# Optimization experiments

Measured on AMD Instinct MI355X. Metric: run time of the kernel, lower is better.

## Reference

```python
import jax, jax.numpy as jnp
import numpy as np

B = 16384      # batch
H = 1024       # latent_dim
C = 2          # output_dim (classes)
PPC = 24       # prototypes per class
P = C * PPC    # 48 total prototypes
EPS = 1e-4


def setup_inputs() -> dict:
    key = jax.random.key(0)
    k1, k2, k3, k4, k5 = jax.random.split(key, 5)
    specific_user = jax.random.normal(k1, (B, H), jnp.float32)
    shared_user = jax.random.normal(k2, (B, H), jnp.float32)
    prototype_vectors = jax.random.normal(k3, (P, H), jnp.float32)
    # last_layer weight set by set_last_layer_incorrect_connection(-0.5):
    # +1 for the prototype's own class, -0.5 elsewhere; shape [C, P]
    cls = np.arange(P) // PPC
    ident = (cls[None, :] == np.arange(C)[:, None]).astype(np.float32)
    last_layer_w = jnp.asarray(ident * 1.0 + (1.0 - ident) * (-0.5))
    # nn.Bilinear(H, H, 1): weight [1, H, H], bias [1]
    bilinear_w = jax.random.normal(k4, (1, H, H), jnp.float32) / np.sqrt(H)
    bilinear_b = jax.random.normal(k5, (1,), jnp.float32) * 0.01
    return {
        "specific_user": specific_user,
        "shared_user": shared_user,
        "prototype_vectors": prototype_vectors,
        "last_layer_w": last_layer_w,
        "bilinear_w": bilinear_w,
        "bilinear_b": bilinear_b,
        "flag": 1,
    }


def reference(specific_user, shared_user, prototype_vectors, last_layer_w,
              bilinear_w, bilinear_b, flag):
    # prototype_distances: squared euclid via mm + norms, then log-similarity
    x2 = jnp.sum(specific_user ** 2, axis=1, keepdims=True)          # [B,1]
    p2 = jnp.sum(prototype_vectors ** 2, axis=1)                     # [P]
    distance = -2.0 * (specific_user @ prototype_vectors.T) + x2 + p2[None, :]  # [B,P]
    similarity = jnp.log((distance + 1.0) / (distance + EPS))        # [B,P]
    logits = similarity @ last_layer_w.T                             # [B,C]

    # select the class's 24 prototypes (flag picks class 1 or 0; static int)
    idx = 1 if flag else 0
    sub = prototype_vectors.reshape(C, PPC, H)[idx]                  # [PPC,H]

    # prototype_subgraph_distances: per original broadcast, each row of
    # all_sim is the batch-mean of the log-similarity -> constant over batch.
    s2 = jnp.sum(sub ** 2, axis=1)                                   # [PPC]
    d = -2.0 * (specific_user @ sub.T) + x2 + s2[None, :]            # [B,PPC]
    sim = jnp.mean(jnp.log((d + 1.0) / (d + EPS)), axis=0)           # [PPC]
    jstar = jnp.argmax(sim)                                          # scalar
    chosen_proto = jnp.broadcast_to(sub[jstar], specific_user.shape) # [B,H]

    # nn.Bilinear(chosen_proto, shared_user) -> [B,1]
    pos = jnp.einsum('bi,ij,bj->b', chosen_proto, bilinear_w[0], shared_user)[:, None] + bilinear_b
    return (pos, shared_user, logits, distance)
```

## Files before the change

### kernel.cpp

```cpp
#include <hip/hip_runtime.h>
#include <hip/hip_bf16.h>

#define BATCH 16384
#define HD    1024
#define NP    48
#define PPC   24
#define EPSV  1e-4f

typedef __attribute__((ext_vector_type(8))) short  short8;
typedef __attribute__((ext_vector_type(4))) float  floatx4;

__device__ __forceinline__ float b2f(unsigned short s) {
    union { unsigned u; float f; } c; c.u = ((unsigned)s) << 16; return c.f;
}
__device__ __forceinline__ unsigned short f2bu(float f) {
    __hip_bfloat16 h = __float2bfloat16(f);
    union { __hip_bfloat16 h; unsigned short u; } c; c.h = h; return c.u;
}

__global__ __launch_bounds__(64) void k_prep(const float* __restrict__ proto,
                                             unsigned short* __restrict__ phi,
                                             unsigned short* __restrict__ plo,
                                             float* __restrict__ p2) {
    const int p = blockIdx.x;
    const int lane = threadIdx.x;
    const float* row = proto + (size_t)p * HD;
    float acc = 0.f;
    for (int k = lane; k < HD; k += 64) {
        const float f = row[k];
        acc += f * f;
        const unsigned short h = f2bu(f);
        phi[(size_t)p * HD + k] = h;
        plo[(size_t)p * HD + k] = f2bu(f - b2f(h));
    }
#pragma unroll
    for (int m = 32; m >= 1; m >>= 1) acc += __shfl_xor(acc, m, 64);
    if (lane == 0) p2[p] = acc;
}

__global__ __launch_bounds__(256, 4) void k_main(
    const float* __restrict__ x,
    const unsigned short* __restrict__ phi,
    const unsigned short* __restrict__ plo,
    const float* __restrict__ llw,
    const float* __restrict__ p2,
    float* __restrict__ gcol,
    float* __restrict__ out_logits,
    float* __restrict__ out_dist)
{
    __shared__ float lacc[4][64][13];
    __shared__ float lx2[4][16];
    const int wave = threadIdx.x >> 6;
    const int lane = threadIdx.x & 63;
    const int quad = lane >> 4;
    const int lr   = lane & 15;
    const int rb   = blockIdx.x * 16;
    const int ko   = wave * 256;

    const float* xr = x + (size_t)(rb + lr) * HD + ko + quad * 8;
    const unsigned short* ph0 = phi + (size_t)lr * HD + ko + quad * 8;
    const unsigned short* ph1 = ph0 + 16 * HD;
    const unsigned short* ph2 = ph0 + 32 * HD;
    const unsigned short* pl0 = plo + (size_t)lr * HD + ko + quad * 8;
    const unsigned short* pl1 = pl0 + 16 * HD;
    const unsigned short* pl2 = pl0 + 32 * HD;

    floatx4 acc0 = {0.f, 0.f, 0.f, 0.f};
    floatx4 acc1 = {0.f, 0.f, 0.f, 0.f};
    floatx4 acc2 = {0.f, 0.f, 0.f, 0.f};
    float x2p = 0.f;

#pragma unroll 2
    for (int kk = 0; kk < 8; ++kk) {
        const floatx4 xa = *(const floatx4*)(xr + kk * 32);
        const floatx4 xb = *(const floatx4*)(xr + kk * 32 + 4);
        short8 ah, al;
#pragma unroll
        for (int j = 0; j < 4; ++j) {
            const float f = xa[j];
            x2p += f * f;
            const unsigned short h = f2bu(f);
            ah[j] = (short)h;
            al[j] = (short)f2bu(f - b2f(h));
        }
#pragma unroll
        for (int j = 0; j < 4; ++j) {
            const float f = xb[j];
            x2p += f * f;
            const unsigned short h = f2bu(f);
            ah[4 + j] = (short)h;
            al[4 + j] = (short)f2bu(f - b2f(h));
        }
        const short8 bh0 = *(const short8*)(ph0 + kk * 32);
        const short8 bh1 = *(const short8*)(ph1 + kk * 32);
        const short8 bh2 = *(const short8*)(ph2 + kk * 32);
        const short8 bl0 = *(const short8*)(pl0 + kk * 32);
        const short8 bl1 = *(const short8*)(pl1 + kk * 32);
        const short8 bl2 = *(const short8*)(pl2 + kk * 32);
        acc0 = __builtin_amdgcn_mfma_f32_16x16x32_bf16(ah, bh0, acc0, 0, 0, 0);
        acc0 = __builtin_amdgcn_mfma_f32_16x16x32_bf16(ah, bl0, acc0, 0, 0, 0);
        acc0 = __builtin_amdgcn_mfma_f32_16x16x32_bf16(al, bh0, acc0, 0, 0, 0);
        acc1 = __builtin_amdgcn_mfma_f32_16x16x32_bf16(ah, bh1, acc1, 0, 0, 0);
        acc1 = __builtin_amdgcn_mfma_f32_16x16x32_bf16(ah, bl1, acc1, 0, 0, 0);
        acc1 = __builtin_amdgcn_mfma_f32_16x16x32_bf16(al, bh1, acc1, 0, 0, 0);
        acc2 = __builtin_amdgcn_mfma_f32_16x16x32_bf16(ah, bh2, acc2, 0, 0, 0);
        acc2 = __builtin_amdgcn_mfma_f32_16x16x32_bf16(ah, bl2, acc2, 0, 0, 0);
        acc2 = __builtin_amdgcn_mfma_f32_16x16x32_bf16(al, bh2, acc2, 0, 0, 0);
    }
    x2p += __shfl_xor(x2p, 16, 64);
    x2p += __shfl_xor(x2p, 32, 64);

#pragma unroll
    for (int r = 0; r < 4; ++r) {
        lacc[wave][lane][r]     = acc0[r];
        lacc[wave][lane][4 + r] = acc1[r];
        lacc[wave][lane][8 + r] = acc2[r];
    }
    if (quad == 0) lx2[wave][lr] = x2p;
    __syncthreads();
    if (wave != 0) return;

    float facc[12];
#pragma unroll
    for (int i = 0; i < 12; ++i)
        facc[i] = lacc[0][lane][i] + lacc[1][lane][i] + lacc[2][lane][i] + lacc[3][lane][i];
    const float x2full = lx2[0][lr] + lx2[1][lr] + lx2[2][lr] + lx2[3][lr];

    float s0[4] = {0.f, 0.f, 0.f, 0.f};
    float s1[4] = {0.f, 0.f, 0.f, 0.f};

#pragma unroll
    for (int t = 0; t < 3; ++t) {
        const int p = t * 16 + lr;
        const float p2p = p2[p];
        const float w0 = llw[p];
        const float w1 = llw[NP + p];
        float cst = 0.f;
#pragma unroll
        for (int r = 0; r < 4; ++r) {
            const int row = quad * 4 + r;
            const float x2r = __shfl(x2full, row, 64);
            const float d = -2.f * facc[t * 4 + r] + x2r + p2p;
            out_dist[(size_t)(rb + row) * NP + p] = d;
            const float sim = log1pf((1.f - EPSV) / (d + EPSV));
            s0[r] += sim * w0;
            s1[r] += sim * w1;
            cst += sim;
        }
        cst += __shfl_xor(cst, 16, 64);
        cst += __shfl_xor(cst, 32, 64);
        if (quad == 0) atomicAdd(&gcol[p], cst);
    }

#pragma unroll
    for (int r = 0; r < 4; ++r) {
        float r0 = s0[r], r1 = s1[r];
#pragma unroll
        for (int m = 1; m <= 8; m <<= 1) {
            r0 += __shfl_xor(r0, m, 64);
            r1 += __shfl_xor(r1, m, 64);
        }
        if (lr == 0) {
            const int brow = rb + quad * 4 + r;
            out_logits[(size_t)brow * 2 + 0] = r0;
            out_logits[(size_t)brow * 2 + 1] = r1;
        }
    }
}

__global__ __launch_bounds__(256) void k_matvec(
    const float* __restrict__ proto,
    const float* __restrict__ w2,
    const float* __restrict__ gcol,
    const int* __restrict__ flag,
    float* __restrict__ v)
{
    __shared__ int js;
    const int tid = threadIdx.x;
    const int idx = (flag[0] != 0) ? 1 : 0;
    if (tid == 0) {
        const float* cs = gcol + idx * PPC;
        int bj = 0; float bv = cs[0];
        for (int j = 1; j < PPC; ++j)
            if (cs[j] > bv) { bv = cs[j]; bj = j; }
        js = bj;
    }
    __syncthreads();

    const float* crow = proto + (size_t)(idx * PPC + js) * HD;
    const int i0 = blockIdx.x * 16;
    const int j4 = tid * 4;
    float a0 = 0.f, a1 = 0.f, a2 = 0.f, a3 = 0.f;
#pragma unroll 4
    for (int i = i0; i < i0 + 16; ++i) {
        const float c = crow[i];
        const floatx4 wv = *(const floatx4*)(w2 + (size_t)i * HD + j4);
        a0 += c * wv[0];
        a1 += c * wv[1];
        a2 += c * wv[2];
        a3 += c * wv[3];
    }
    atomicAdd(&v[j4 + 0], a0);
    atomicAdd(&v[j4 + 1], a1);
    atomicAdd(&v[j4 + 2], a2);
    atomicAdd(&v[j4 + 3], a3);
}

__global__ __launch_bounds__(256) void k_pos(
    const float* __restrict__ sh,
    const float* __restrict__ v,
    const float* __restrict__ bias,
    float* __restrict__ out_pos,
    float* __restrict__ out_copy)
{
    const int wave = threadIdx.x >> 6;
    const int lane = threadIdx.x & 63;
    const int b = blockIdx.x * 4 + wave;

    const floatx4* src = (const floatx4*)(sh + (size_t)b * HD);
    floatx4* dst = (floatx4*)(out_copy + (size_t)b * HD);
    const floatx4* vv = (const floatx4*)v;
    float acc = 0.f;
#pragma unroll
    for (int c = 0; c < 4; ++c) {
        const int idx = c * 64 + lane;
        const floatx4 r = src[idx];
        __builtin_nontemporal_store(r, &dst[idx]);
        const floatx4 vr = vv[idx];
#pragma unroll
        for (int j = 0; j < 4; ++j) acc += r[j] * vr[j];
    }
#pragma unroll
    for (int m = 1; m <= 32; m <<= 1) acc += __shfl_xor(acc, m, 64);
    if (lane == 0) out_pos[b] = acc + bias[0];
}

extern "C" void kernel_launch(void* const* d_in, const int* in_sizes, int n_in,
                              void* d_out, int out_size, void* d_ws, size_t ws_size,
                              hipStream_t stream) {
    const float* x     = (const float*)d_in[0];
    const float* sh    = (const float*)d_in[1];
    const float* proto = (const float*)d_in[2];
    const float* llw   = (const float*)d_in[3];
    const float* w2    = (const float*)d_in[4];
    const float* bb    = (const float*)d_in[5];
    const int*   flag  = (const int*)d_in[6];

    float* out = (float*)d_out;
    float* out_pos    = out;
    float* out_copy   = out + BATCH;
    float* out_logits = out + BATCH + BATCH * HD;
    float* out_dist   = out + BATCH + BATCH * HD + BATCH * 2;

    float* ws_v    = (float*)d_ws;
    float* ws_col  = ws_v + 1024;
    float* ws_p2   = ws_v + 1088;
    unsigned short* ws_phi = (unsigned short*)(ws_v + 16384);
    unsigned short* ws_plo = ws_phi + NP * HD;

    hipMemsetAsync(d_ws, 0, 8192, stream);
    k_prep<<<48, 64, 0, stream>>>(proto, ws_phi, ws_plo, ws_p2);
    k_main<<<1024, 256, 0, stream>>>(x, ws_phi, ws_plo, llw, ws_p2, ws_col, out_logits, out_dist);
    k_matvec<<<64, 256, 0, stream>>>(proto, w2, ws_col, flag, ws_v);
    k_pos<<<4096, 256, 0, stream>>>(sh, ws_v, bb, out_pos, out_copy);
}
```

Measured before the change: 228.8 us.

## Fold workspace zeroing into prep, preload x rows, widen matvec grid

Removes the separate hipMemsetAsync by having block 0 of the prep kernel zero the accumulators, and vectorizes the prep kernel to 256 threads with short4 stores. The main kernel now loads all 16 float4 slices of x up front into registers and fully unrolls the K loop, with launch bounds relaxed to 2 blocks per CU to allow the extra registers. The matvec kernel is split over 256 blocks of 4 rows instead of 64 blocks of 16 rows to spread the bilinear weight read across more CUs, at the cost of more atomics.

```diff
diff --git a/kernel.cpp b/kernel.cpp
--- a/kernel.cpp
+++ b/kernel.cpp
@@ -18,27 +18,40 @@
     union { __hip_bfloat16 h; unsigned short u; } c; c.h = h; return c.u;
 }
 
-__global__ __launch_bounds__(64) void k_prep(const float* __restrict__ proto,
-                                             unsigned short* __restrict__ phi,
-                                             unsigned short* __restrict__ plo,
-                                             float* __restrict__ p2) {
-    const int p = blockIdx.x;
-    const int lane = threadIdx.x;
-    const float* row = proto + (size_t)p * HD;
+__global__ __launch_bounds__(256) void k_prep(const float* __restrict__ proto,
+                                              unsigned short* __restrict__ phi,
+                                              unsigned short* __restrict__ plo,
+                                              float* __restrict__ p2,
+                                              float* __restrict__ ws_v,
+                                              float* __restrict__ ws_col) {
+    const int p   = blockIdx.x;
+    const int tid = threadIdx.x;
+    if (p == 0) {
+        floatx4 z = {0.f, 0.f, 0.f, 0.f};
+        ((floatx4*)ws_v)[tid] = z;
+        if (tid < NP) ws_col[tid] = 0.f;
+    }
+    const floatx4 f4 = *(const floatx4*)(proto + (size_t)p * HD + tid * 4);
     float acc = 0.f;
-    for (int k = lane; k < HD; k += 64) {
-        const float f = row[k];
+    unsigned short hs[4], ls[4];
+#pragma unroll
+    for (int j = 0; j < 4; ++j) {
+        const float f = f4[j];
         acc += f * f;
-        const unsigned short h = f2bu(f);
-        phi[(size_t)p * HD + k] = h;
-        plo[(size_t)p * HD + k] = f2bu(f - b2f(h));
-    }
+        hs[j] = f2bu(f);
+        ls[j] = f2bu(f - b2f(hs[j]));
+    }
+    *(short4*)(void*)(phi + (size_t)p * HD + tid * 4) = make_short4(hs[0], hs[1], hs[2], hs[3]);
+    *(short4*)(void*)(plo + (size_t)p * HD + tid * 4) = make_short4(ls[0], ls[1], ls[2], ls[3]);
 #pragma unroll
     for (int m = 32; m >= 1; m >>= 1) acc += __shfl_xor(acc, m, 64);
-    if (lane == 0) p2[p] = acc;
-}
-
-__global__ __launch_bounds__(256, 4) void k_main(
+    __shared__ float ws[4];
+    if ((tid & 63) == 0) ws[tid >> 6] = acc;
+    __syncthreads();
+    if (tid == 0) p2[p] = ws[0] + ws[1] + ws[2] + ws[3];
+}
+
+__global__ __launch_bounds__(256, 2) void k_main(
     const float* __restrict__ x,
     const unsigned short* __restrict__ phi,
     const unsigned short* __restrict__ plo,
@@ -58,6 +71,14 @@
     const int ko   = wave * 256;
 
     const float* xr = x + (size_t)(rb + lr) * HD + ko + quad * 8;
+
+    floatx4 xv[16];
+#pragma unroll
+    for (int kk = 0; kk < 8; ++kk) {
+        xv[2 * kk]     = *(const floatx4*)(xr + kk * 32);
+        xv[2 * kk + 1] = *(const floatx4*)(xr + kk * 32 + 4);
+    }
+
     const unsigned short* ph0 = phi + (size_t)lr * HD + ko + quad * 8;
     const unsigned short* ph1 = ph0 + 16 * HD;
     const unsigned short* ph2 = ph0 + 32 * HD;
@@ -70,26 +91,20 @@
     floatx4 acc2 = {0.f, 0.f, 0.f, 0.f};
     float x2p = 0.f;
 
-#pragma unroll 2
+#pragma unroll
     for (int kk = 0; kk < 8; ++kk) {
-        const floatx4 xa = *(const floatx4*)(xr + kk * 32);
-        const floatx4 xb = *(const floatx4*)(xr + kk * 32 + 4);
         short8 ah, al;
 #pragma unroll
-        for (int j = 0; j < 4; ++j) {
-            const float f = xa[j];
-            x2p += f * f;
-            const unsigned short h = f2bu(f);
-            ah[j] = (short)h;
-            al[j] = (short)f2bu(f - b2f(h));
-        }
-#pragma unroll
-        for (int j = 0; j < 4; ++j) {
-            const float f = xb[j];
-            x2p += f * f;
-            const unsigned short h = f2bu(f);
-            ah[4 + j] = (short)h;
-            al[4 + j] = (short)f2bu(f - b2f(h));
+        for (int half = 0; half < 2; ++half) {
+            const floatx4 xa = xv[2 * kk + half];
+#pragma unroll
+            for (int j = 0; j < 4; ++j) {
+                const float f = xa[j];
+                x2p += f * f;
+                const unsigned short h = f2bu(f);
+                ah[half * 4 + j] = (short)h;
+                al[half * 4 + j] = (short)f2bu(f - b2f(h));
+            }
         }
         const short8 bh0 = *(const short8*)(ph0 + kk * 32);
         const short8 bh1 = *(const short8*)(ph1 + kk * 32);
@@ -188,11 +203,11 @@
     __syncthreads();
 
     const float* crow = proto + (size_t)(idx * PPC + js) * HD;
-    const int i0 = blockIdx.x * 16;
+    const int i0 = blockIdx.x * 4;
     const int j4 = tid * 4;
     float a0 = 0.f, a1 = 0.f, a2 = 0.f, a3 = 0.f;
-#pragma unroll 4
-    for (int i = i0; i < i0 + 16; ++i) {
+#pragma unroll
+    for (int i = i0; i < i0 + 4; ++i) {
         const float c = crow[i];
         const floatx4 wv = *(const floatx4*)(w2 + (size_t)i * HD + j4);
         a0 += c * wv[0];
@@ -258,9 +273,8 @@
     unsigned short* ws_phi = (unsigned short*)(ws_v + 16384);
     unsigned short* ws_plo = ws_phi + NP * HD;
 
-    hipMemsetAsync(d_ws, 0, 8192, stream);
-    k_prep<<<48, 64, 0, stream>>>(proto, ws_phi, ws_plo, ws_p2);
+    k_prep<<<48, 256, 0, stream>>>(proto, ws_phi, ws_plo, ws_p2, ws_v, ws_col);
     k_main<<<1024, 256, 0, stream>>>(x, ws_phi, ws_plo, llw, ws_p2, ws_col, out_logits, out_dist);
-    k_matvec<<<64, 256, 0, stream>>>(proto, w2, ws_col, flag, ws_v);
+    k_matvec<<<256, 256, 0, stream>>>(proto, w2, ws_col, flag, ws_v);
     k_pos<<<4096, 256, 0, stream>>>(sh, ws_v, bb, out_pos, out_copy);
 }
```

Measured after the change: 243.9 us. 6.6% more time.
